# Kernel optimization log

Hardware: AMD Instinct MI355X
Metric: run time of the kernel (lower is better)

The kernel has to match this reference:

```python
import jax, jax.numpy as jnp
import numpy as np

MAX_NODES = 32
PHYSICS_MARGIN = 0.1
BATCH = 16384


def setup_inputs() -> dict:
    key = jax.random.key(0)
    k1, k2, k3 = jax.random.split(key, 3)
    eps = 1e-6
    # predicted probabilities in (0,1)
    pred_A = jnp.clip(jax.random.uniform(k1, (BATCH, MAX_NODES, MAX_NODES), dtype=jnp.float32), eps, 1.0 - eps)
    # binary 0/1 target adjacency
    target_A = (jax.random.uniform(k2, (BATCH, MAX_NODES, MAX_NODES), dtype=jnp.float32) < 0.3).astype(jnp.float32)
    # per-graph node counts in [8, 32]; mask first n nodes
    n_nodes = jax.random.randint(k3, (BATCH, 1), 8, MAX_NODES + 1)
    node_mask = (jnp.arange(MAX_NODES)[None, :] < n_nodes).astype(jnp.float32)
    return {"pred_A": pred_A, "target_A": target_A, "node_mask": node_mask}


def reference(pred_A, target_A, node_mask):
    # masked, sum-reduced BCE normalized by number of valid entries
    mask_2d = node_mask[:, :, None] * node_mask[:, None, :]  # [B, N, N]
    bce = -(target_A * jnp.log(pred_A) + (1.0 - target_A) * jnp.log(1.0 - pred_A))
    bce_loss = jnp.sum(bce * mask_2d) / jnp.maximum(jnp.sum(mask_2d), 1.0)

    # Laplacian L = D - A with increasing diagonal jitter for numerical safety
    D_diag = jnp.sum(pred_A, axis=-1)  # [B, N]
    jitter = jnp.linspace(1e-5, 1e-4, MAX_NODES, dtype=pred_A.dtype)
    L_safe = jnp.apply_along_axis(jnp.diag, -1, np.zeros(1)) if False else None  # placeholder avoided
    L_safe = -pred_A
    idx = jnp.arange(MAX_NODES)
    L_safe = L_safe.at[:, idx, idx].add(D_diag + jitter)  # D - A + jitter on diagonal

    eigenvalues = jnp.linalg.eigvalsh(L_safe)  # ascending, [B, N]
    lambda_2 = eigenvalues[:, 1]
    physics_loss = jnp.mean(jax.nn.relu(PHYSICS_MARGIN - lambda_2))

    return (bce_loss, physics_loss, jax.lax.stop_gradient(lambda_2))
```

## Files before the change

### kernel.cpp

```cpp
#include <hip/hip_runtime.h>
#include <math.h>

#define NB 32
#define BATCH 16384
#define WPB 4
#define TPB (WPB * 64)


template<int CTRL>
__device__ __forceinline__ float dpp_add(float v) {
    const int s = __float_as_int(v);
    const int r = __builtin_amdgcn_update_dpp(s, s, CTRL, 0xF, 0xF, false);
    return v + __int_as_float(r);
}
template<int CTRL>
__device__ __forceinline__ float dpp_min(float v) {
    const int s = __float_as_int(v);
    const int r = __builtin_amdgcn_update_dpp(s, s, CTRL, 0xF, 0xF, false);
    return fminf(v, __int_as_float(r));
}
template<int CTRL>
__device__ __forceinline__ float dpp_max(float v) {
    const int s = __float_as_int(v);
    const int r = __builtin_amdgcn_update_dpp(s, s, CTRL, 0xF, 0xF, false);
    return fmaxf(v, __int_as_float(r));
}
__device__ __forceinline__ float pair_sum(float v) { return dpp_add<0xB1>(v); }
__device__ __forceinline__ float wave64_sum(float v) {
    v = dpp_add<0x121>(v); v = dpp_add<0x122>(v);
    v = dpp_add<0x124>(v); v = dpp_add<0x128>(v);
    v += __shfl_xor(v, 16, 64);
    v += __shfl_xor(v, 32, 64);
    return v;
}
__device__ __forceinline__ float wave64_min(float v) {
    v = dpp_min<0x121>(v); v = dpp_min<0x122>(v);
    v = dpp_min<0x124>(v); v = dpp_min<0x128>(v);
    v = fminf(v, __shfl_xor(v, 16, 64));
    return fminf(v, __shfl_xor(v, 32, 64));
}
__device__ __forceinline__ float wave64_max(float v) {
    v = dpp_max<0x121>(v); v = dpp_max<0x122>(v);
    v = dpp_max<0x124>(v); v = dpp_max<0x128>(v);
    v = fmaxf(v, __shfl_xor(v, 16, 64));
    return fmaxf(v, __shfl_xor(v, 32, 64));
}

__global__ __launch_bounds__(TPB)
void lap_main(const float* __restrict__ predA, const float* __restrict__ targA,
              const float* __restrict__ nmask, float* __restrict__ out,
              float* __restrict__ ws)
{
    __shared__ float  sv[WPB][NB];
    __shared__ float  sp[WPB][NB];
    __shared__ float2 sde[WPB][NB];
    __shared__ float  red[WPB][3];

    const int t = threadIdx.x;
    const int w = t >> 6;
    const int l = t & 63;
    const int r = l >> 1;
    const int h = l & 1;
    const int b = blockIdx.x * WPB + w;
    const size_t base = (size_t)b * (NB * NB);

    const float  mr  = nmask[(size_t)b * NB + r];
    const float4* pr4 = (const float4*)(predA + base + (size_t)r * NB + 16 * h);
    const float4* tr4 = (const float4*)(targA + base + (size_t)r * NB + 16 * h);
    const float4* nm4 = (const float4*)(nmask + (size_t)b * NB + 16 * h);

    float a[16];
    float accB = 0.f, accM = 0.f;
    #pragma unroll
    for (int q = 0; q < 4; ++q) {
        const float4 p  = pr4[q];
        const float4 tg = tr4[q];
        const float4 mc = nm4[q];
        const float bx = -(tg.x * __logf(p.x) + (1.f - tg.x) * __logf(1.f - p.x));
        const float by = -(tg.y * __logf(p.y) + (1.f - tg.y) * __logf(1.f - p.y));
        const float bz = -(tg.z * __logf(p.z) + (1.f - tg.z) * __logf(1.f - p.z));
        const float bw = -(tg.w * __logf(p.w) + (1.f - tg.w) * __logf(1.f - p.w));
        accB += mr * (mc.x * bx + mc.y * by + mc.z * bz + mc.w * bw);
        accM += mr * (mc.x + mc.y + mc.z + mc.w);
        a[4*q+0] = p.x; a[4*q+1] = p.y; a[4*q+2] = p.z; a[4*q+3] = p.w;
    }

    float dsl = 0.f, pdl = 0.f;
    #pragma unroll
    for (int u = 0; u < 16; ++u) {
        dsl += a[u];
        pdl = (16 * h + u == r) ? a[u] : pdl;
    }
    const float dsum  = pair_sum(dsl);
    const float pdiag = pair_sum((16 * h + ((r & 15)) == r) ? 0.f : 0.f) * 0.f + pair_sum(pdl);
    const float jitter = 1e-5f + (9e-5f / 31.f) * (float)r;
    const float dval = dsum + jitter - pdiag;
    #pragma unroll
    for (int q = 0; q < 4; ++q) {
        #pragma unroll
        for (int u = 0; u < 4; ++u) {
            const int cl = 4 * q + u;
            const int c  = 16 * h + cl;
            const float cv = predA[base + (size_t)c * NB + r];
            a[cl] = (c == r) ? dval : -0.5f * (a[cl] + cv);
        }
    }

    {
        const float cap0 = (h == 0) ? a[0] : 0.f;
        float ck = pair_sum(cap0);
        a[0] = a[0];
        (void)ck;
    }
    float colk;
    {
        const float cap0 = (h == 0) ? a[0] : 0.f;
        colk = pair_sum(cap0);
    }

    const float4* v4h = (const float4*)&sv[w][16 * h];
    const float4* p4h = (const float4*)&sp[w][16 * h];
    for (int k = 0; k < NB - 2; ++k) {
        const float sg = wave64_sum((h == 0 && r > k) ? colk * colk : 0.f);
        const float x1 = __shfl(colk, 2 * (k + 1), 64);
        const float al = (x1 >= 0.f) ? -sqrtf(sg) : sqrtf(sg);
        const float denom = sg - al * x1;
        const float beta  = (denom > 1e-30f) ? __builtin_amdgcn_rcpf(denom) : 0.f;
        const float vj = (r > k) ? (colk - ((r == k + 1) ? al : 0.f)) : 0.f;
        if (h == 0) sv[w][r] = vj;

        float ac0 = 0.f, ac1 = 0.f, ac2 = 0.f, ac3 = 0.f;
        #pragma unroll
        for (int q = 0; q < 4; ++q) {
            if (16 + 4 * q + 3 >= k) {
                const float4 x = v4h[q];
                ac0 += a[4*q+0] * x.x;
                ac1 += a[4*q+1] * x.y;
                ac2 += a[4*q+2] * x.z;
                ac3 += a[4*q+3] * x.w;
            }
        }
        const float dhalf = (ac0 + ac1) + (ac2 + ac3);
        const float dot = pair_sum(dhalf);
        const float pj  = beta * dot;
        const float pjm = (r >= k) ? pj : 0.f;
        if (h == 0) sp[w][r] = pjm;
        const float K  = wave64_sum((h == 0) ? vj * pjm : 0.f);
        const float c2 = 0.5f * beta * K;
        const float s2 = pjm - 2.f * c2 * vj;
        const float nv = -vj, ns = -s2;

        float cap = 0.f;
        if (r >= k) {
            #pragma unroll
            for (int q = 0; q < 4; ++q) {
                if (16 + 4 * q + 3 >= k) {
                    const float4 x4 = v4h[q];
                    const float4 p4 = p4h[q];
                    #pragma unroll
                    for (int u = 0; u < 4; ++u) {
                        const int cl = 4 * q + u;
                        const float xv = (u==0)?x4.x:(u==1)?x4.y:(u==2)?x4.z:x4.w;
                        const float pv = (u==0)?p4.x:(u==1)?p4.y:(u==2)?p4.z:p4.w;
                        float av = a[cl];
                        av = fmaf(nv, pv, av);
                        av = fmaf(ns, xv, av);
                        a[cl] = av;
                        cap = (16 * h + cl == k + 1) ? av : cap;
                    }
                }
            }
        }
        colk = pair_sum(cap);
    }

    float dl = 0.f, el = 0.f;
    #pragma unroll
    for (int u = 0; u < 16; ++u) {
        dl = (16 * h + u == r)     ? a[u] : dl;
        el = (16 * h + u == r - 1) ? a[u] : el;
    }
    const float d = pair_sum(dl);
    const float e = pair_sum(el);
    if (h == 0) sde[w][r] = make_float2(d, e * e);

    const float ae  = fabsf(e);
    const float aen = (r == 31) ? 0.f : __shfl(ae, (l + 2) & 63, 64);
    float lo = wave64_min(d - (ae + aen));
    float hi = wave64_max(d + (ae + aen));

    const float2* de = (const float2*)&sde[w][0];
    for (int round = 0; round < 3; ++round) {
        asm volatile("" ::: "memory");
        const float step = (hi - lo) * (1.f / 65.f);
        const float sig = lo + step * (float)(l + 1);
        float q = de[0].x - sig;
        int cnt = (q < 0.f);
        #pragma unroll
        for (int i = 1; i < NB; ++i) {
            const float2 di = de[i];
            if (fabsf(q) < 1e-20f) q = (q < 0.f) ? -1e-20f : 1e-20f;
            q = (di.x - sig) - di.y * __builtin_amdgcn_rcpf(q);
            cnt += (q < 0.f);
        }
        const unsigned long long bal = __ballot(cnt >= 2);
        const int jstar = (bal == 0ull) ? 64 : __builtin_ctzll(bal);
        const float nlo = lo + step * (float)jstar;
        const float nhi = lo + step * (float)(jstar + 1);
        lo = nlo; hi = nhi;
    }
    const float lam2 = 0.5f * (lo + hi);

    if (l == 0) out[2 + b] = lam2;

    const float accBs = wave64_sum(accB);
    const float accMs = wave64_sum(accM);
    const float ph = fmaxf(0.1f - lam2, 0.f);
    if (l == 0) { red[w][0] = accBs; red[w][1] = accMs; red[w][2] = ph; }
    __syncthreads();
    if (t == 0) {
        float sB = 0.f, sM = 0.f, sP = 0.f;
        #pragma unroll
        for (int i = 0; i < WPB; ++i) { sB += red[i][0]; sM += red[i][1]; sP += red[i][2]; }
        atomicAdd(ws + 0, sB);
        atomicAdd(ws + 1, sM);
        atomicAdd(ws + 2, sP);
    }
}

__global__ __launch_bounds__(64)
void lap_final(float* __restrict__ out, const float* __restrict__ ws) {
    if (threadIdx.x == 0) {
        out[0] = ws[0] / fmaxf(ws[1], 1.f);
        out[1] = ws[2] * (1.f / (float)BATCH);
    }
}

extern "C" void kernel_launch(void* const* d_in, const int* in_sizes, int n_in,
                              void* d_out, int out_size, void* d_ws, size_t ws_size,
                              hipStream_t stream) {
    const float* pred = (const float*)d_in[0];
    const float* targ = (const float*)d_in[1];
    const float* nm   = (const float*)d_in[2];
    float* out = (float*)d_out;
    float* ws  = (float*)d_ws;

    (void)hipMemsetAsync(d_ws, 0, 16, stream);
    hipLaunchKernelGGL(lap_main, dim3(BATCH / WPB), dim3(TPB), 0, stream,
                       pred, targ, nm, out, ws);
    hipLaunchKernelGGL(lap_final, dim3(1), dim3(64), 0, stream, out, ws);
}
```

Measured before the change: 357.7 us.

## Process two graphs per wavefront to interleave independent Householder chains

Each wavefront now handles two batch matrices at once, running both tridiagonalization and bisection chains interleaved so independent reductions, shuffles and LDS accesses can hide each other's latency. The grid is halved accordingly and launch bounds request occupancy of 4 blocks. This trades doubled register use per thread, and so possibly fewer resident waves, for more instruction-level parallelism in the serial, latency-bound reduction loops.

```diff
diff --git a/kernel.cpp b/kernel.cpp
--- a/kernel.cpp
+++ b/kernel.cpp
@@ -5,6 +5,7 @@
 #define BATCH 16384
 #define WPB 4
 #define TPB (WPB * 64)
+#define MPB (WPB * 2)
 
 
 template<int CTRL>
@@ -46,14 +47,14 @@
     return fmaxf(v, __shfl_xor(v, 32, 64));
 }
 
-__global__ __launch_bounds__(TPB)
+__global__ __launch_bounds__(TPB, 4)
 void lap_main(const float* __restrict__ predA, const float* __restrict__ targA,
               const float* __restrict__ nmask, float* __restrict__ out,
               float* __restrict__ ws)
 {
-    __shared__ float  sv[WPB][NB];
-    __shared__ float  sp[WPB][NB];
-    __shared__ float2 sde[WPB][NB];
+    __shared__ float  svA_[WPB][NB], svB_[WPB][NB];
+    __shared__ float  spA_[WPB][NB], spB_[WPB][NB];
+    __shared__ float2 sdeA_[WPB][NB], sdeB_[WPB][NB];
     __shared__ float  red[WPB][3];
 
     const int t = threadIdx.x;
@@ -61,161 +62,218 @@
     const int l = t & 63;
     const int r = l >> 1;
     const int h = l & 1;
-    const int b = blockIdx.x * WPB + w;
-    const size_t base = (size_t)b * (NB * NB);
-
-    const float  mr  = nmask[(size_t)b * NB + r];
-    const float4* pr4 = (const float4*)(predA + base + (size_t)r * NB + 16 * h);
-    const float4* tr4 = (const float4*)(targA + base + (size_t)r * NB + 16 * h);
-    const float4* nm4 = (const float4*)(nmask + (size_t)b * NB + 16 * h);
-
-    float a[16];
+    const int bA = blockIdx.x * MPB + w * 2;
+    const int bB = bA + 1;
+    const size_t baseA = (size_t)bA * (NB * NB);
+    const size_t baseB = (size_t)bB * (NB * NB);
+
+    const float mrA = nmask[(size_t)bA * NB + r];
+    const float mrB = nmask[(size_t)bB * NB + r];
+    const float4* prA = (const float4*)(predA + baseA + (size_t)r * NB + 16 * h);
+    const float4* trA = (const float4*)(targA + baseA + (size_t)r * NB + 16 * h);
+    const float4* nmA = (const float4*)(nmask + (size_t)bA * NB + 16 * h);
+    const float4* prB = (const float4*)(predA + baseB + (size_t)r * NB + 16 * h);
+    const float4* trB = (const float4*)(targA + baseB + (size_t)r * NB + 16 * h);
+    const float4* nmB = (const float4*)(nmask + (size_t)bB * NB + 16 * h);
+
+    float aA[16], aB[16];
     float accB = 0.f, accM = 0.f;
     #pragma unroll
     for (int q = 0; q < 4; ++q) {
-        const float4 p  = pr4[q];
-        const float4 tg = tr4[q];
-        const float4 mc = nm4[q];
+        const float4 p  = prA[q];
+        const float4 tg = trA[q];
+        const float4 mc = nmA[q];
         const float bx = -(tg.x * __logf(p.x) + (1.f - tg.x) * __logf(1.f - p.x));
         const float by = -(tg.y * __logf(p.y) + (1.f - tg.y) * __logf(1.f - p.y));
         const float bz = -(tg.z * __logf(p.z) + (1.f - tg.z) * __logf(1.f - p.z));
         const float bw = -(tg.w * __logf(p.w) + (1.f - tg.w) * __logf(1.f - p.w));
-        accB += mr * (mc.x * bx + mc.y * by + mc.z * bz + mc.w * bw);
-        accM += mr * (mc.x + mc.y + mc.z + mc.w);
-        a[4*q+0] = p.x; a[4*q+1] = p.y; a[4*q+2] = p.z; a[4*q+3] = p.w;
-    }
-
-    float dsl = 0.f, pdl = 0.f;
+        accB += mrA * (mc.x * bx + mc.y * by + mc.z * bz + mc.w * bw);
+        accM += mrA * (mc.x + mc.y + mc.z + mc.w);
+        aA[4*q+0] = p.x; aA[4*q+1] = p.y; aA[4*q+2] = p.z; aA[4*q+3] = p.w;
+    }
+    #pragma unroll
+    for (int q = 0; q < 4; ++q) {
+        const float4 p  = prB[q];
+        const float4 tg = trB[q];
+        const float4 mc = nmB[q];
+        const float bx = -(tg.x * __logf(p.x) + (1.f - tg.x) * __logf(1.f - p.x));
+        const float by = -(tg.y * __logf(p.y) + (1.f - tg.y) * __logf(1.f - p.y));
+        const float bz = -(tg.z * __logf(p.z) + (1.f - tg.z) * __logf(1.f - p.z));
+        const float bw = -(tg.w * __logf(p.w) + (1.f - tg.w) * __logf(1.f - p.w));
+        accB += mrB * (mc.x * bx + mc.y * by + mc.z * bz + mc.w * bw);
+        accM += mrB * (mc.x + mc.y + mc.z + mc.w);
+        aB[4*q+0] = p.x; aB[4*q+1] = p.y; aB[4*q+2] = p.z; aB[4*q+3] = p.w;
+    }
+
+    float dslA = 0.f, pdlA = 0.f, dslB = 0.f, pdlB = 0.f;
     #pragma unroll
     for (int u = 0; u < 16; ++u) {
-        dsl += a[u];
-        pdl = (16 * h + u == r) ? a[u] : pdl;
-    }
-    const float dsum  = pair_sum(dsl);
-    const float pdiag = pair_sum((16 * h + ((r & 15)) == r) ? 0.f : 0.f) * 0.f + pair_sum(pdl);
+        dslA += aA[u]; pdlA = (16 * h + u == r) ? aA[u] : pdlA;
+        dslB += aB[u]; pdlB = (16 * h + u == r) ? aB[u] : pdlB;
+    }
     const float jitter = 1e-5f + (9e-5f / 31.f) * (float)r;
-    const float dval = dsum + jitter - pdiag;
-    #pragma unroll
-    for (int q = 0; q < 4; ++q) {
-        #pragma unroll
-        for (int u = 0; u < 4; ++u) {
-            const int cl = 4 * q + u;
-            const int c  = 16 * h + cl;
-            const float cv = predA[base + (size_t)c * NB + r];
-            a[cl] = (c == r) ? dval : -0.5f * (a[cl] + cv);
-        }
-    }
-
+    const float dvA = pair_sum(dslA) + jitter - pair_sum(pdlA);
+    const float dvB = pair_sum(dslB) + jitter - pair_sum(pdlB);
+    #pragma unroll
+    for (int u = 0; u < 16; ++u) {
+        const int c = 16 * h + u;
+        const float cvA = predA[baseA + (size_t)c * NB + r];
+        const float cvB = predA[baseB + (size_t)c * NB + r];
+        aA[u] = (c == r) ? dvA : -0.5f * (aA[u] + cvA);
+        aB[u] = (c == r) ? dvB : -0.5f * (aB[u] + cvB);
+    }
+
+    float colA, colB;
     {
-        const float cap0 = (h == 0) ? a[0] : 0.f;
-        float ck = pair_sum(cap0);
-        a[0] = a[0];
-        (void)ck;
-    }
-    float colk;
-    {
-        const float cap0 = (h == 0) ? a[0] : 0.f;
-        colk = pair_sum(cap0);
-    }
-
-    const float4* v4h = (const float4*)&sv[w][16 * h];
-    const float4* p4h = (const float4*)&sp[w][16 * h];
+        const float c0A = (h == 0) ? aA[0] : 0.f;
+        const float c0B = (h == 0) ? aB[0] : 0.f;
+        colA = pair_sum(c0A);
+        colB = pair_sum(c0B);
+    }
+
+    float* svA = &svA_[w][0]; float* svB = &svB_[w][0];
+    float* spA = &spA_[w][0]; float* spB = &spB_[w][0];
+    const float4* vA4 = (const float4*)&svA[16 * h];
+    const float4* vB4 = (const float4*)&svB[16 * h];
+    const float4* pA4 = (const float4*)&spA[16 * h];
+    const float4* pB4 = (const float4*)&spB[16 * h];
     for (int k = 0; k < NB - 2; ++k) {
-        const float sg = wave64_sum((h == 0 && r > k) ? colk * colk : 0.f);
-        const float x1 = __shfl(colk, 2 * (k + 1), 64);
-        const float al = (x1 >= 0.f) ? -sqrtf(sg) : sqrtf(sg);
-        const float denom = sg - al * x1;
-        const float beta  = (denom > 1e-30f) ? __builtin_amdgcn_rcpf(denom) : 0.f;
-        const float vj = (r > k) ? (colk - ((r == k + 1) ? al : 0.f)) : 0.f;
-        if (h == 0) sv[w][r] = vj;
-
-        float ac0 = 0.f, ac1 = 0.f, ac2 = 0.f, ac3 = 0.f;
+        const float sgA = wave64_sum((h == 0 && r > k) ? colA * colA : 0.f);
+        const float sgB = wave64_sum((h == 0 && r > k) ? colB * colB : 0.f);
+        const float x1A = __shfl(colA, 2 * (k + 1), 64);
+        const float x1B = __shfl(colB, 2 * (k + 1), 64);
+        const float alA = (x1A >= 0.f) ? -sqrtf(sgA) : sqrtf(sgA);
+        const float alB = (x1B >= 0.f) ? -sqrtf(sgB) : sqrtf(sgB);
+        const float deA = sgA - alA * x1A;
+        const float deB = sgB - alB * x1B;
+        const float beA = (deA > 1e-30f) ? __builtin_amdgcn_rcpf(deA) : 0.f;
+        const float beB = (deB > 1e-30f) ? __builtin_amdgcn_rcpf(deB) : 0.f;
+        const float vjA = (r > k) ? (colA - ((r == k + 1) ? alA : 0.f)) : 0.f;
+        const float vjB = (r > k) ? (colB - ((r == k + 1) ? alB : 0.f)) : 0.f;
+        if (h == 0) { svA[r] = vjA; svB[r] = vjB; }
+
+        float a0 = 0.f, a1 = 0.f, a2 = 0.f, a3 = 0.f;
+        float b0 = 0.f, b1 = 0.f, b2 = 0.f, b3 = 0.f;
         #pragma unroll
         for (int q = 0; q < 4; ++q) {
             if (16 + 4 * q + 3 >= k) {
-                const float4 x = v4h[q];
-                ac0 += a[4*q+0] * x.x;
-                ac1 += a[4*q+1] * x.y;
-                ac2 += a[4*q+2] * x.z;
-                ac3 += a[4*q+3] * x.w;
+                const float4 xA = vA4[q];
+                const float4 xB = vB4[q];
+                a0 += aA[4*q+0] * xA.x; a1 += aA[4*q+1] * xA.y;
+                a2 += aA[4*q+2] * xA.z; a3 += aA[4*q+3] * xA.w;
+                b0 += aB[4*q+0] * xB.x; b1 += aB[4*q+1] * xB.y;
+                b2 += aB[4*q+2] * xB.z; b3 += aB[4*q+3] * xB.w;
             }
         }
-        const float dhalf = (ac0 + ac1) + (ac2 + ac3);
-        const float dot = pair_sum(dhalf);
-        const float pj  = beta * dot;
-        const float pjm = (r >= k) ? pj : 0.f;
-        if (h == 0) sp[w][r] = pjm;
-        const float K  = wave64_sum((h == 0) ? vj * pjm : 0.f);
-        const float c2 = 0.5f * beta * K;
-        const float s2 = pjm - 2.f * c2 * vj;
-        const float nv = -vj, ns = -s2;
-
-        float cap = 0.f;
+        const float dotA = pair_sum((a0 + a1) + (a2 + a3));
+        const float dotB = pair_sum((b0 + b1) + (b2 + b3));
+        const float pjA = beA * dotA;
+        const float pjB = beB * dotB;
+        const float pmA = (r >= k) ? pjA : 0.f;
+        const float pmB = (r >= k) ? pjB : 0.f;
+        if (h == 0) { spA[r] = pmA; spB[r] = pmB; }
+        const float KA = wave64_sum((h == 0) ? vjA * pmA : 0.f);
+        const float KB = wave64_sum((h == 0) ? vjB * pmB : 0.f);
+        const float s2A = pmA - 2.f * (0.5f * beA * KA) * vjA;
+        const float s2B = pmB - 2.f * (0.5f * beB * KB) * vjB;
+        const float nvA = -vjA, nsA = -s2A;
+        const float nvB = -vjB, nsB = -s2B;
+
+        float capA = 0.f, capB = 0.f;
         if (r >= k) {
             #pragma unroll
             for (int q = 0; q < 4; ++q) {
                 if (16 + 4 * q + 3 >= k) {
-                    const float4 x4 = v4h[q];
-                    const float4 p4 = p4h[q];
+                    const float4 xA = vA4[q]; const float4 pA = pA4[q];
+                    const float4 xB = vB4[q]; const float4 pB = pB4[q];
                     #pragma unroll
                     for (int u = 0; u < 4; ++u) {
                         const int cl = 4 * q + u;
-                        const float xv = (u==0)?x4.x:(u==1)?x4.y:(u==2)?x4.z:x4.w;
-                        const float pv = (u==0)?p4.x:(u==1)?p4.y:(u==2)?p4.z:p4.w;
-                        float av = a[cl];
-                        av = fmaf(nv, pv, av);
-                        av = fmaf(ns, xv, av);
-                        a[cl] = av;
-                        cap = (16 * h + cl == k + 1) ? av : cap;
+                        const float xvA = (u==0)?xA.x:(u==1)?xA.y:(u==2)?xA.z:xA.w;
+                        const float pvA = (u==0)?pA.x:(u==1)?pA.y:(u==2)?pA.z:pA.w;
+                        const float xvB = (u==0)?xB.x:(u==1)?xB.y:(u==2)?xB.z:xB.w;
+                        const float pvB = (u==0)?pB.x:(u==1)?pB.y:(u==2)?pB.z:pB.w;
+                        float vA = aA[cl];
+                        vA = fmaf(nvA, pvA, vA);
+                        vA = fmaf(nsA, xvA, vA);
+                        aA[cl] = vA;
+                        float vB = aB[cl];
+                        vB = fmaf(nvB, pvB, vB);
+                        vB = fmaf(nsB, xvB, vB);
+                        aB[cl] = vB;
+                        capA = (16 * h + cl == k + 1) ? vA : capA;
+                        capB = (16 * h + cl == k + 1) ? vB : capB;
                     }
                 }
             }
         }
-        colk = pair_sum(cap);
-    }
-
-    float dl = 0.f, el = 0.f;
+        colA = pair_sum(capA);
+        colB = pair_sum(capB);
+    }
+
+    float dlA = 0.f, elA = 0.f, dlB = 0.f, elB = 0.f;
     #pragma unroll
     for (int u = 0; u < 16; ++u) {
-        dl = (16 * h + u == r)     ? a[u] : dl;
-        el = (16 * h + u == r - 1) ? a[u] : el;
-    }
-    const float d = pair_sum(dl);
-    const float e = pair_sum(el);
-    if (h == 0) sde[w][r] = make_float2(d, e * e);
-
-    const float ae  = fabsf(e);
-    const float aen = (r == 31) ? 0.f : __shfl(ae, (l + 2) & 63, 64);
-    float lo = wave64_min(d - (ae + aen));
-    float hi = wave64_max(d + (ae + aen));
-
-    const float2* de = (const float2*)&sde[w][0];
+        dlA = (16 * h + u == r)     ? aA[u] : dlA;
+        elA = (16 * h + u == r - 1) ? aA[u] : elA;
+        dlB = (16 * h + u == r)     ? aB[u] : dlB;
+        elB = (16 * h + u == r - 1) ? aB[u] : elB;
+    }
+    const float dA = pair_sum(dlA);
+    const float eA = pair_sum(elA);
+    const float dB = pair_sum(dlB);
+    const float eB = pair_sum(elB);
+    if (h == 0) { sdeA_[w][r] = make_float2(dA, eA * eA);
+                  sdeB_[w][r] = make_float2(dB, eB * eB); }
+
+    const float aeA = fabsf(eA), aeB = fabsf(eB);
+    const float anA = (r == 31) ? 0.f : __shfl(aeA, (l + 2) & 63, 64);
+    const float anB = (r == 31) ? 0.f : __shfl(aeB, (l + 2) & 63, 64);
+    float loA = wave64_min(dA - (aeA + anA));
+    float hiA = wave64_max(dA + (aeA + anA));
+    float loB = wave64_min(dB - (aeB + anB));
+    float hiB = wave64_max(dB + (aeB + anB));
+
+    const float2* deA = (const float2*)&sdeA_[w][0];
+    const float2* deB = (const float2*)&sdeB_[w][0];
     for (int round = 0; round < 3; ++round) {
         asm volatile("" ::: "memory");
-        const float step = (hi - lo) * (1.f / 65.f);
-        const float sig = lo + step * (float)(l + 1);
-        float q = de[0].x - sig;
-        int cnt = (q < 0.f);
+        const float stA = (hiA - loA) * (1.f / 65.f);
+        const float stB = (hiB - loB) * (1.f / 65.f);
+        const float siA = loA + stA * (float)(l + 1);
+        const float siB = loB + stB * (float)(l + 1);
+        float qA = deA[0].x - siA;
+        float qB = deB[0].x - siB;
+        int cA = (qA < 0.f), cB = (qB < 0.f);
         #pragma unroll
         for (int i = 1; i < NB; ++i) {
-            const float2 di = de[i];
-            if (fabsf(q) < 1e-20f) q = (q < 0.f) ? -1e-20f : 1e-20f;
-            q = (di.x - sig) - di.y * __builtin_amdgcn_rcpf(q);
-            cnt += (q < 0.f);
+            const float2 diA = deA[i];
+            const float2 diB = deB[i];
+            if (fabsf(qA) < 1e-20f) qA = (qA < 0.f) ? -1e-20f : 1e-20f;
+            if (fabsf(qB) < 1e-20f) qB = (qB < 0.f) ? -1e-20f : 1e-20f;
+            qA = (diA.x - siA) - diA.y * __builtin_amdgcn_rcpf(qA);
+            qB = (diB.x - siB) - diB.y * __builtin_amdgcn_rcpf(qB);
+            cA += (qA < 0.f);
+            cB += (qB < 0.f);
         }
-        const unsigned long long bal = __ballot(cnt >= 2);
-        const int jstar = (bal == 0ull) ? 64 : __builtin_ctzll(bal);
-        const float nlo = lo + step * (float)jstar;
-        const float nhi = lo + step * (float)(jstar + 1);
-        lo = nlo; hi = nhi;
-    }
-    const float lam2 = 0.5f * (lo + hi);
-
-    if (l == 0) out[2 + b] = lam2;
+        const unsigned long long balA = __ballot(cA >= 2);
+        const unsigned long long balB = __ballot(cB >= 2);
+        const int jsA = (balA == 0ull) ? 64 : __builtin_ctzll(balA);
+        const int jsB = (balB == 0ull) ? 64 : __builtin_ctzll(balB);
+        const float nlA = loA + stA * (float)jsA;
+        const float nhA = loA + stA * (float)(jsA + 1);
+        const float nlB = loB + stB * (float)jsB;
+        const float nhB = loB + stB * (float)(jsB + 1);
+        loA = nlA; hiA = nhA; loB = nlB; hiB = nhB;
+    }
+    const float lamA = 0.5f * (loA + hiA);
+    const float lamB = 0.5f * (loB + hiB);
+
+    if (l == 0) { out[2 + bA] = lamA; out[2 + bB] = lamB; }
 
     const float accBs = wave64_sum(accB);
     const float accMs = wave64_sum(accM);
-    const float ph = fmaxf(0.1f - lam2, 0.f);
+    const float ph = fmaxf(0.1f - lamA, 0.f) + fmaxf(0.1f - lamB, 0.f);
     if (l == 0) { red[w][0] = accBs; red[w][1] = accMs; red[w][2] = ph; }
     __syncthreads();
     if (t == 0) {
@@ -246,7 +304,7 @@
     float* ws  = (float*)d_ws;
 
     (void)hipMemsetAsync(d_ws, 0, 16, stream);
-    hipLaunchKernelGGL(lap_main, dim3(BATCH / WPB), dim3(TPB), 0, stream,
+    hipLaunchKernelGGL(lap_main, dim3(BATCH / MPB), dim3(TPB), 0, stream,
                        pred, targ, nm, out, ws);
     hipLaunchKernelGGL(lap_final, dim3(1), dim3(64), 0, stream, out, ws);
 }
```

New measurement: 336.9 us. -5.8%, faster.
